# Optimization experiments

Hardware: AMD Instinct MI355X
Metric: run time of the kernel (lower is better)

## Reference

```python
import jax, jax.numpy as jnp
import numpy as np

PAD = 26
H = 1900
B = 256
T_EPI = 25
T_ANT = 64
T_TOT = 153
EMB = 10
IC = 2 * H  # classifier in_channels = 3800


def setup_inputs() -> dict:
    key = jax.random.key(0)
    ks = jax.random.split(key, 16)
    def rn(i, s, sc):
        return jax.random.normal(ks[i], s, jnp.float32) * sc
    inp = {
        "epitope_x": jax.random.randint(ks[0], (B, T_EPI), 0, 26),
        "left_antigen_x": jax.random.randint(ks[1], (B, T_ANT), 0, 26),
        "right_antigen_x": jax.random.randint(ks[2], (B, T_ANT), 0, 26),
        "total_antigen_x": jax.random.randint(ks[3], (B, T_TOT), 0, 26),
        "embed": rn(4, (27, EMB), 0.1),
        "wx": rn(5, (EMB, 4 * H), 0.1),
        "wh": rn(6, (H, 4 * H), 0.02),
        "wmx": rn(7, (EMB, H), 0.1),
        "wmh": rn(8, (H, H), 0.02),
        "b": rn(9, (4 * H,), 0.1),
        "gx": jnp.ones((4 * H,), jnp.float32),
        "gh": jnp.ones((4 * H,), jnp.float32),
        "gmx": jnp.ones((H,), jnp.float32),
        "gmh": jnp.ones((H,), jnp.float32),
        "bn1_gamma": jnp.ones((IC,), jnp.float32),
        "bn1_beta": jnp.zeros((IC,), jnp.float32),
        "bn1_mean": jnp.zeros((IC,), jnp.float32),
        "bn1_var": jnp.ones((IC,), jnp.float32),
        "W1": rn(10, (IC, IC // 10), 0.02),
        "b1": jnp.zeros((IC // 10,), jnp.float32),
        "bn2_gamma": jnp.ones((IC // 10,), jnp.float32),
        "bn2_beta": jnp.zeros((IC // 10,), jnp.float32),
        "bn2_mean": jnp.zeros((IC // 10,), jnp.float32),
        "bn2_var": jnp.ones((IC // 10,), jnp.float32),
        "W2": rn(11, (IC // 10, 1), 0.05),
        "b2": jnp.zeros((1,), jnp.float32),
    }
    return inp


def _wn(w, g):
    # tf.nn.l2_normalize(w, dim=0) * g  (eps 1e-12)
    return w * (g * jax.lax.rsqrt(jnp.maximum(jnp.sum(w * w, axis=0, keepdims=True), 1e-12)))


def _mlstm(xs, wx, wh, wmx, wmh, b):
    # xs: [T, B, E] -> hidden states [B, T, H]
    nB = xs.shape[1]
    def step(carry, x):
        c, h = carry
        m = (x @ wmx) * (h @ wmh)
        z = x @ wx + m @ wh + b
        i, f, o, u = jnp.split(z, 4, axis=1)
        c = jax.nn.sigmoid(f) * c + jax.nn.sigmoid(i) * jnp.tanh(u)
        h = jax.nn.sigmoid(o) * jnp.tanh(c)
        return (c, h), h
    init = (jnp.zeros((nB, H), xs.dtype), jnp.zeros((nB, H), xs.dtype))
    _, hs = jax.lax.scan(step, init, xs)
    return jnp.swapaxes(hs, 0, 1)


def _forward(epitope_x, left_antigen_x, right_antigen_x, total_antigen_x, embed,
             wx, wh, wmx, wmh, b, gx, gh, gmx, gmh,
             bn1_gamma, bn1_beta, bn1_mean, bn1_var, W1, b1,
             bn2_gamma, bn2_beta, bn2_mean, bn2_var, W2, b2):
    wxn = _wn(wx, gx); whn = _wn(wh, gh); wmxn = _wn(wmx, gmx); wmhn = _wn(wmh, gmh)
    epi_len = jnp.sum((epitope_x != PAD).astype(jnp.int32), axis=1)
    left_len = jnp.maximum(jnp.sum((left_antigen_x != PAD).astype(jnp.int32), axis=1), 1)
    right_len = jnp.maximum(jnp.sum((right_antigen_x != PAD).astype(jnp.int32), axis=1), 1)
    tot_len = epi_len + left_len + right_len
    epi_emb = embed[epitope_x]          # [B, 25, 10]
    tot_emb = embed[total_antigen_x]    # [B, 153, 10]
    epi_hs = _mlstm(jnp.swapaxes(epi_emb, 0, 1), wxn, whn, wmxn, wmhn, b)   # [B, 25, H]
    tot_hs = _mlstm(jnp.swapaxes(tot_emb, 0, 1), wxn, whn, wmxn, wmhn, b)   # [B, 153, H]
    ei = jnp.clip(epi_len - 1, 0, epi_hs.shape[1] - 1)
    ti = jnp.clip(tot_len - 1, 0, tot_hs.shape[1] - 1)
    epi_h = jnp.take_along_axis(epi_hs, ei[:, None, None], axis=1)[:, 0]
    tot_h = jnp.take_along_axis(tot_hs, ti[:, None, None], axis=1)[:, 0]
    x = jnp.concatenate([tot_h, epi_h], axis=-1)  # [B, 3800]
    lrelu = lambda v: jnp.where(v >= 0, v, 0.3 * v)
    bn = lambda v, g, bt, m, vv: (v - m) * jax.lax.rsqrt(vv + 1e-3) * g + bt
    x = bn(lrelu(x), bn1_gamma, bn1_beta, bn1_mean, bn1_var)
    x = x @ W1 + b1
    x = bn(lrelu(x), bn2_gamma, bn2_beta, bn2_mean, bn2_var)
    x = x @ W2 + b2
    return x.reshape(-1)


def reference(epitope_x, left_antigen_x, right_antigen_x, total_antigen_x, embed,
              wx, wh, wmx, wmh, b, gx, gh, gmx, gmh,
              bn1_gamma, bn1_beta, bn1_mean, bn1_var, W1, b1,
              bn2_gamma, bn2_beta, bn2_mean, bn2_var, W2, b2):
    return _forward(epitope_x, left_antigen_x, right_antigen_x, total_antigen_x, embed,
                    wx, wh, wmx, wmh, b, gx, gh, gmx, gmh,
                    bn1_gamma, bn1_beta, bn1_mean, bn1_var, W1, b1,
                    bn2_gamma, bn2_beta, bn2_mean, bn2_var, W2, b2)
```

## Files before the change

kernel.cpp:

```cpp
#include <hip/hip_runtime.h>


typedef _Float16 f16;
typedef _Float16 half8 __attribute__((ext_vector_type(8)));
typedef float f32x4 __attribute__((ext_vector_type(4)));

#define H_    1900
#define HP    1920
#define NKA   60
#define NKB   61
#define NKF   120
#define NR    512
#define TT    153
#define TE    25
#define EMB_  10
#define FCN   384

__device__ __forceinline__ float sigm(float x) {
  float p = __expf(-fabsf(x));
  float r = 1.f / (1.f + p);
  return x >= 0.f ? r : 1.f - r;
}
__device__ __forceinline__ float tanh_(float x) {
  float p = __expf(-2.f * fabsf(x));
  float r = (1.f - p) / (1.f + p);
  return x >= 0.f ? r : -r;
}

__device__ __forceinline__ void gll16(const f16* g, f16* l) {
  __builtin_amdgcn_global_load_lds(
      (const __attribute__((address_space(1))) unsigned int*)g,
      (__attribute__((address_space(3))) unsigned int*)l, 16, 0, 0);
}


__global__ void k_norms_p(const float* __restrict__ wh, const float* __restrict__ wx,
                          const float* __restrict__ wmh, const float* __restrict__ wmx,
                          float* __restrict__ part) {
  int seg = blockIdx.x & 3;
  int tid = (blockIdx.x >> 2) * 256 + threadIdx.x;
  float s = 0.f;
  if (tid < 7600) {
    int k0 = seg * 475;
    for (int k = k0; k < k0 + 475; k++) { float v = wh[(size_t)k * 7600 + tid]; s += v * v; }
  } else if (tid < 15200) {
    if (seg == 0) {
      int n = tid - 7600;
      for (int e = 0; e < EMB_; e++) { float v = wx[(size_t)e * 7600 + n]; s += v * v; }
    }
  } else if (tid < 17100) {
    int n = tid - 15200; int k0 = seg * 475;
    for (int k = k0; k < k0 + 475; k++) { float v = wmh[(size_t)k * H_ + n]; s += v * v; }
  } else if (tid < 19000) {
    if (seg == 0) {
      int n = tid - 17100;
      for (int e = 0; e < EMB_; e++) { float v = wmx[(size_t)e * H_ + n]; s += v * v; }
    }
  }
  if (tid < 19000) part[(size_t)seg * 19000 + tid] = s;
}

__global__ void k_norms_f(const float* __restrict__ part,
                          const float* __restrict__ gh, const float* __restrict__ gx,
                          const float* __restrict__ gmh, const float* __restrict__ gmx,
                          float* __restrict__ inv_wh, float* __restrict__ inv_wx,
                          float* __restrict__ inv_wmh, float* __restrict__ inv_wmx) {
  int tid = blockIdx.x * 256 + threadIdx.x;
  if (tid >= 19000) return;
  float s = part[tid] + part[19000 + tid] + part[38000 + tid] + part[57000 + tid];
  float r = rsqrtf(fmaxf(s, 1e-12f));
  if (tid < 7600)        inv_wh[tid] = gh[tid] * r;
  else if (tid < 15200)  { int n = tid - 7600;  inv_wx[n]  = gx[n]  * r; }
  else if (tid < 17100)  { int n = tid - 15200; inv_wmh[n] = gmh[n] * r; }
  else                   { int n = tid - 17100; inv_wmx[n] = gmx[n] * r; }
}

__global__ void k_wmhS(const float* __restrict__ wmh, const float* __restrict__ inv,
                       f16* __restrict__ WmhS) {
  int i = blockIdx.x * 256 + threadIdx.x;
  if (i >= 1920 * 1920) return;
  int n = i % 1920, k = i / 1920;
  float v = (n < H_ && k < H_) ? wmh[(size_t)k * H_ + n] * inv[n] : 0.f;
  int c = n >> 4, nl = n & 15, kb = k >> 5, kl = k & 31;
  WmhS[(((size_t)c * NKA + kb) * 512) + (nl + 16 * (kl >> 3)) * 8 + (kl & 7)] = (f16)v;
}

__global__ void k_whS(const float* __restrict__ wh, const float* __restrict__ wx,
                      const float* __restrict__ bias,
                      const float* __restrict__ inv_wh, const float* __restrict__ inv_wx,
                      f16* __restrict__ WhS) {
  int i = blockIdx.x * 256 + threadIdx.x;
  if (i >= 7600 * 1952) return;
  int col = i % 7600, k = i / 7600;
  float v = 0.f;
  if (k < H_)                        v = wh[(size_t)k * 7600 + col] * inv_wh[col];
  else if (k >= HP && k < HP + EMB_) v = wx[(size_t)(k - HP) * 7600 + col] * inv_wx[col];
  else if (k == HP + EMB_)           v = bias[col];
  int g = col / H_, n = col % H_;
  int q = n >> 4, nl = n & 15, kb = k >> 5, kl = k & 31;
  WhS[(((size_t)(q * 4 + g) * NKB + kb) * 512) + (nl + 16 * (kl >> 3)) * 8 + (kl & 7)] = (f16)v;
}

__global__ void k_wmxT(const float* __restrict__ wmx, const float* __restrict__ inv_wmx,
                       f16* __restrict__ wmxT) {
  int i = blockIdx.x * 256 + threadIdx.x;
  if (i >= HP * 32) return;
  int n = i >> 5, k = i & 31;
  float v = (k < EMB_ && n < H_) ? wmx[(size_t)k * H_ + n] * inv_wmx[n] : 0.f;
  wmxT[i] = (f16)v;
}

__global__ void k_lens(const int* __restrict__ ex, const int* __restrict__ lx,
                       const int* __restrict__ rx, int* __restrict__ sel) {
  int s = threadIdx.x;
  int el = 0; for (int i = 0; i < 25; i++) el += (ex[s * 25 + i] != 26);
  int ll = 0; for (int i = 0; i < 64; i++) ll += (lx[s * 64 + i] != 26);
  int rl = 0; for (int i = 0; i < 64; i++) rl += (rx[s * 64 + i] != 26);
  ll = ll < 1 ? 1 : ll;  rl = rl < 1 ? 1 : rl;
  int tl = el + ll + rl;
  int ti = tl - 1; ti = ti < 0 ? 0 : (ti > 152 ? 152 : ti);
  int ei = el - 1; ei = ei < 0 ? 0 : (ei > 24 ? 24 : ei);
  sel[s] = ti; sel[256 + s] = ei;
}

__global__ void k_init(f16* __restrict__ h0, f16* __restrict__ h1, float* __restrict__ c) {
  int i = blockIdx.x * 256 + threadIdx.x;
  if (i < NR * HP) { h0[i] = (f16)0.f; h1[i] = (f16)0.f; c[i] = 0.f; }
}

__global__ void k_xe16(const int* __restrict__ totx, const int* __restrict__ epix,
                       const float* __restrict__ embed, f16* __restrict__ xe16) {
  int i = blockIdx.x * blockDim.x + threadIdx.x;
  if (i >= TT * NR) return;
  int t = i / NR, r = i % NR;
  int tok = -1;
  if (r < 256) tok = totx[r * TT + t];
  else if (t < TE) tok = epix[(r - 256) * TE + t];
  f16* o = xe16 + (size_t)i * 32;
  #pragma unroll
  for (int e = 0; e < EMB_; e++) o[e] = (f16)(tok >= 0 ? embed[tok * EMB_ + e] : 0.f);
  o[10] = (f16)1.f;
  #pragma unroll
  for (int e = 11; e < 32; e++) o[e] = (f16)0.f;
}


__global__ __launch_bounds__(256, 2)
void k_stepA(const f16* __restrict__ hS, const f16* __restrict__ WmhS,
             const f16* __restrict__ xe16_t, const f16* __restrict__ wmxT,
             f16* __restrict__ mS, int rgc) {
  __shared__ __align__(16) f16 Bb[2][8][2][512];
  const int lane = threadIdx.x & 63, wid = threadIdx.x >> 6;
  const int bi = blockIdx.x;
  const int x = bi & 7, mm = bi >> 3;
  const int rg = mm % rgc, rem = mm / rgc;
  const int cbh = rem & 1, chi = rem >> 1;
  const int ct = chi * 8 + x;
  if (ct >= 30) return;
  const int rtile = rg * 4 + wid;
  const int r0 = rtile * 16;
  const int l16 = lane & 15, l4 = lane >> 4;

  const f16* Abase = hS   + (size_t)rtile * NKA * 512 + lane * 8;
  const f16* Bglob = WmhS + (size_t)(ct * 4 + cbh * 2) * NKA * 512 + lane * 8;

  f32x4 xm[2];
  {
    half8 xa = *(const half8*)(xe16_t + (size_t)(r0 + l16) * 32 + l4 * 8);
    #pragma unroll
    for (int cb = 0; cb < 2; cb++) {
      half8 xb = *(const half8*)(wmxT + (size_t)(ct * 64 + (cbh * 2 + cb) * 16 + l16) * 32 + l4 * 8);
      f32x4 z = {0.f, 0.f, 0.f, 0.f};
      xm[cb] = __builtin_amdgcn_mfma_f32_16x16x32_f16(xa, xb, z, 0, 0, 0);
    }
  }

  half8 Areg[2][8];
  f32x4 acc[2];
  #pragma unroll
  for (int cb = 0; cb < 2; cb++) { f32x4 z = {0.f, 0.f, 0.f, 0.f}; acc[cb] = z; }

#define STAGE_A(g, buf, n_) { _Pragma("unroll") for (int q_ = 0; q_ < ((n_) >> 1); q_++) { \
    int p_ = wid * ((n_) >> 1) + q_; int kbl_ = p_ >> 1, cb_ = p_ & 1; \
    gll16(Bglob + ((size_t)cb_ * NKA + (g) * 8 + kbl_) * 512, &Bb[buf][kbl_][cb_][0]); } }
#define LOADA_A(g, buf, n_) { _Pragma("unroll") for (int kk_ = 0; kk_ < 8; kk_++) if (kk_ < (n_)) \
    Areg[buf][kk_] = *(const half8*)(Abase + (size_t)((g) * 8 + kk_) * 512); }
#define COMP_A(g, buf, n_) { _Pragma("unroll") for (int kk_ = 0; kk_ < 8; kk_++) if (kk_ < (n_)) { \
    half8 b0_ = *(const half8*)&Bb[buf][kk_][0][lane * 8]; \
    half8 b1_ = *(const half8*)&Bb[buf][kk_][1][lane * 8]; \
    acc[0] = __builtin_amdgcn_mfma_f32_16x16x32_f16(Areg[buf][kk_], b0_, acc[0], 0, 0, 0); \
    acc[1] = __builtin_amdgcn_mfma_f32_16x16x32_f16(Areg[buf][kk_], b1_, acc[1], 0, 0, 0); } }

  LOADA_A(0, 0, 8); STAGE_A(0, 0, 8);
  __syncthreads();
  #pragma unroll
  for (int g = 0; g < 8; g++) {
    const int nn = (g == 7) ? 4 : 8;
    if (g < 7) {
      const int nn1 = (g == 6) ? 4 : 8;
      STAGE_A(g + 1, (g + 1) & 1, nn1); LOADA_A(g + 1, (g + 1) & 1, nn1);
    }
    COMP_A(g, g & 1, nn);
    __syncthreads();
  }
#undef STAGE_A
#undef LOADA_A
#undef COMP_A

  const int q4 = lane >> 4, c16 = lane & 15;
  const int kb = ct * 2 + cbh;
  #pragma unroll
  for (int cb = 0; cb < 2; cb++) {
    int klane = cb * 16 + c16;
    int lf = (klane >> 3) * 16;
    int sub = c16 & 7;
    f16* dst = mS + ((size_t)rtile * NKB + kb) * 512 + sub;
    #pragma unroll
    for (int q = 0; q < 4; q++) {
      int rl = q4 * 4 + q;
      dst[(rl + lf) * 8] = (f16)(acc[cb][q] * xm[cb][q]);
    }
  }
  if (ct == 0 && cbh == 0) {
    f16* dst = mS + ((size_t)rtile * NKB + 60) * 512 + lane * 8;
    *(half8*)dst = *(const half8*)(xe16_t + (size_t)(r0 + l16) * 32 + l4 * 8);
  }
}

__global__ __launch_bounds__(256, 2)
void k_stepB(const f16* __restrict__ mS, const f16* __restrict__ WhS,
             float* __restrict__ c, f16* __restrict__ houtS,
             float* __restrict__ selH, const int* __restrict__ sel, int t, int rgc) {
  __shared__ __align__(16) f16 Bb[2][4][4][512];
  const int lane = threadIdx.x & 63, wid = threadIdx.x >> 6;
  const int bi = blockIdx.x;
  const int x = bi & 7, mm = bi >> 3;
  const int rg = mm % rgc, chi = mm / rgc;
  const int colq = chi * 8 + x;
  if (colq >= 119) return;
  const int rtile = rg * 4 + wid;
  const int r0 = rtile * 16;

  const f16* Abase = mS  + (size_t)rtile * NKB * 512 + lane * 8;
  const f16* Bglob = WhS + (size_t)(colq * 4) * NKB * 512 + lane * 8;

  half8 Areg[2][4];
  f32x4 acc[4];
  #pragma unroll
  for (int b = 0; b < 4; b++) { f32x4 z = {0.f, 0.f, 0.f, 0.f}; acc[b] = z; }

#define STAGE_B(g, buf, n_) { _Pragma("unroll") for (int q_ = 0; q_ < (n_); q_++) { \
    int p_ = wid * (n_) + q_; int kbl_ = p_ >> 2, gg_ = p_ & 3; \
    gll16(Bglob + ((size_t)gg_ * NKB + (g) * 4 + kbl_) * 512, &Bb[buf][kbl_][gg_][0]); } }
#define LOADA_B(g, buf, n_) { _Pragma("unroll") for (int kk_ = 0; kk_ < 4; kk_++) if (kk_ < (n_)) \
    Areg[buf][kk_] = *(const half8*)(Abase + (size_t)((g) * 4 + kk_) * 512); }
#define COMP_B(g, buf, n_) { _Pragma("unroll") for (int kk_ = 0; kk_ < 4; kk_++) if (kk_ < (n_)) { \
    half8 b0_ = *(const half8*)&Bb[buf][kk_][0][lane * 8]; \
    half8 b1_ = *(const half8*)&Bb[buf][kk_][1][lane * 8]; \
    half8 b2_ = *(const half8*)&Bb[buf][kk_][2][lane * 8]; \
    half8 b3_ = *(const half8*)&Bb[buf][kk_][3][lane * 8]; \
    acc[0] = __builtin_amdgcn_mfma_f32_16x16x32_f16(Areg[buf][kk_], b0_, acc[0], 0, 0, 0); \
    acc[1] = __builtin_amdgcn_mfma_f32_16x16x32_f16(Areg[buf][kk_], b1_, acc[1], 0, 0, 0); \
    acc[2] = __builtin_amdgcn_mfma_f32_16x16x32_f16(Areg[buf][kk_], b2_, acc[2], 0, 0, 0); \
    acc[3] = __builtin_amdgcn_mfma_f32_16x16x32_f16(Areg[buf][kk_], b3_, acc[3], 0, 0, 0); } }

  LOADA_B(0, 0, 4); STAGE_B(0, 0, 4);
  __syncthreads();
  #pragma unroll
  for (int g = 0; g < 16; g++) {
    const int nn = (g == 15) ? 1 : 4;
    if (g < 15) {
      const int nn1 = (g == 14) ? 1 : 4;
      STAGE_B(g + 1, (g + 1) & 1, nn1); LOADA_B(g + 1, (g + 1) & 1, nn1);
    }
    COMP_B(g, g & 1, nn);
    __syncthreads();
  }
#undef STAGE_B
#undef LOADA_B
#undef COMP_B

  const int q4 = lane >> 4, c16 = lane & 15;
  const int j = colq * 16 + c16;
  const bool valid = j < H_;
  const int kbh = colq >> 1;
  const int lfh = ((((colq & 1) * 16 + c16) >> 3)) * 16;
  const int subh = c16 & 7;
  f16* hdst = houtS + ((size_t)rtile * NKA + kbh) * 512 + subh;
  #pragma unroll
  for (int q = 0; q < 4; q++) {
    int rl = q4 * 4 + q;
    int row = r0 + rl;
    if (valid) {
      size_t idx = (size_t)row * HP + j;
      float cold = c[idx];
      float iz = acc[0][q], fz = acc[1][q];
      float oz = acc[2][q], uz = acc[3][q];
      float cn = sigm(fz) * cold + sigm(iz) * tanh_(uz);
      float hv = sigm(oz) * tanh_(cn);
      c[idx] = cn;
      hdst[(rl + lfh) * 8] = (f16)hv;
      if (t == sel[row]) selH[idx] = hv;
    }
  }
}


__global__ void k_xqS(const float* __restrict__ selH, const float* __restrict__ g1,
                      const float* __restrict__ be1, const float* __restrict__ mu1,
                      const float* __restrict__ var1, f16* __restrict__ xqS) {
  int i = blockIdx.x * 256 + threadIdx.x;
  if (i >= 256 * 3840) return;
  int k = i % 3840, s = i / 3840;
  float v = 0.f; bool have = false;
  if (k < H_)            { v = selH[(size_t)s * HP + k]; have = true; }
  else if (k < 2 * H_)   { v = selH[(size_t)(256 + s) * HP + (k - H_)]; have = true; }
  float q = 0.f;
  if (have) {
    float lr = v < 0.f ? 0.3f * v : v;
    q = (lr - mu1[k]) * rsqrtf(var1[k] + 1e-3f) * g1[k] + be1[k];
  }
  int rtile = s >> 4, sl = s & 15, kb = k >> 5, kl = k & 31;
  xqS[(((size_t)rtile * NKF + kb) * 512) + (sl + 16 * (kl >> 3)) * 8 + (kl & 7)] = (f16)q;
}

__global__ void k_w1S(const float* __restrict__ W1, f16* __restrict__ W1S) {
  int i = blockIdx.x * 256 + threadIdx.x;
  if (i >= 384 * 3840) return;
  int col = i % 384, k = i / 384;
  float v = (col < 380 && k < 2 * H_) ? W1[(size_t)k * 380 + col] : 0.f;
  int cg = col >> 4, nl = col & 15, kb = k >> 5, kl = k & 31;
  W1S[(((size_t)cg * NKF + kb) * 512) + (nl + 16 * (kl >> 3)) * 8 + (kl & 7)] = (f16)v;
}

__global__ __launch_bounds__(256)
void k_fc1(const f16* __restrict__ xqS, const f16* __restrict__ W1S,
           const float* __restrict__ b1, float* __restrict__ z1) {
  const int lane = threadIdx.x & 63, wid = threadIdx.x >> 6;
  const int ct = blockIdx.x % 6, rg = blockIdx.x / 6;
  const int rtile = rg * 4 + wid;
  const int r0 = rtile * 16;

  const f16* Abase = xqS + (size_t)rtile * NKF * 512 + lane * 8;
  const f16* Bbase = W1S + (size_t)(ct * 4) * NKF * 512 + lane * 8;

  half8 fa0, fa1, fa2, fa3;
  half8 fb0[4], fb1[4], fb2[4], fb3[4];
  f32x4 acc[4];
  #pragma unroll
  for (int cb = 0; cb < 4; cb++) { f32x4 z = {0.f, 0.f, 0.f, 0.f}; acc[cb] = z; }

#define LDA_F(d, kb)  d = *(const half8*)(Abase + (size_t)(kb) * 512)
#define LDB_F(d, kb)  { _Pragma("unroll") for (int cb = 0; cb < 4; cb++) \
    d[cb] = *(const half8*)(Bbase + ((size_t)cb * NKF + (kb)) * 512); }
#define MMA_F(fa, fb) { _Pragma("unroll") for (int cb = 0; cb < 4; cb++) \
    acc[cb] = __builtin_amdgcn_mfma_f32_16x16x32_f16(fa, fb[cb], acc[cb], 0, 0, 0); }

  LDA_F(fa0, 0); LDB_F(fb0, 0);
  LDA_F(fa1, 1); LDB_F(fb1, 1);
  LDA_F(fa2, 2); LDB_F(fb2, 2);
  for (int base = 0; base < 116; base += 4) {
    LDA_F(fa3, base + 3); LDB_F(fb3, base + 3);
    MMA_F(fa0, fb0);
    LDA_F(fa0, base + 4); LDB_F(fb0, base + 4);
    MMA_F(fa1, fb1);
    LDA_F(fa1, base + 5); LDB_F(fb1, base + 5);
    MMA_F(fa2, fb2);
    LDA_F(fa2, base + 6); LDB_F(fb2, base + 6);
    MMA_F(fa3, fb3);
  }
  LDA_F(fa3, 119); LDB_F(fb3, 119);
  MMA_F(fa0, fb0);
  MMA_F(fa1, fb1);
  MMA_F(fa2, fb2);
  MMA_F(fa3, fb3);
#undef LDA_F
#undef LDB_F
#undef MMA_F

  const int q4 = lane >> 4, c16 = lane & 15;
  #pragma unroll
  for (int cb = 0; cb < 4; cb++)
    #pragma unroll
    for (int q = 0; q < 4; q++) {
      int row = r0 + q4 * 4 + q;
      int col = ct * 64 + cb * 16 + c16;
      float bias = (col < 380) ? b1[col] : 0.f;
      z1[(size_t)row * FCN + col] = acc[cb][q] + bias;
    }
}

__global__ void k_fc2(const float* __restrict__ z1, const float* __restrict__ g2,
                      const float* __restrict__ be2, const float* __restrict__ mu2,
                      const float* __restrict__ var2, const float* __restrict__ W2,
                      const float* __restrict__ b2, float* __restrict__ out) {
  int s = threadIdx.x;
  float a = 0.f;
  for (int jj = 0; jj < 380; jj++) {
    float v = z1[(size_t)s * FCN + jj];
    float lr = v < 0.f ? 0.3f * v : v;
    float q = (lr - mu2[jj]) * rsqrtf(var2[jj] + 1e-3f) * g2[jj] + be2[jj];
    a += q * W2[jj];
  }
  out[s] = a + b2[0];
}


extern "C" void kernel_launch(void* const* d_in, const int* in_sizes, int n_in,
                              void* d_out, int out_size, void* d_ws, size_t ws_size,
                              hipStream_t stream) {
  const int*   epix  = (const int*)d_in[0];
  const int*   lx    = (const int*)d_in[1];
  const int*   rx    = (const int*)d_in[2];
  const int*   totx  = (const int*)d_in[3];
  const float* embed = (const float*)d_in[4];
  const float* wx    = (const float*)d_in[5];
  const float* wh    = (const float*)d_in[6];
  const float* wmx   = (const float*)d_in[7];
  const float* wmh   = (const float*)d_in[8];
  const float* bb    = (const float*)d_in[9];
  const float* gx    = (const float*)d_in[10];
  const float* gh    = (const float*)d_in[11];
  const float* gmx   = (const float*)d_in[12];
  const float* gmh   = (const float*)d_in[13];
  const float* bn1g  = (const float*)d_in[14];
  const float* bn1b  = (const float*)d_in[15];
  const float* bn1m  = (const float*)d_in[16];
  const float* bn1v  = (const float*)d_in[17];
  const float* W1    = (const float*)d_in[18];
  const float* b1    = (const float*)d_in[19];
  const float* bn2g  = (const float*)d_in[20];
  const float* bn2b  = (const float*)d_in[21];
  const float* bn2m  = (const float*)d_in[22];
  const float* bn2v  = (const float*)d_in[23];
  const float* W2    = (const float*)d_in[24];
  const float* b2v   = (const float*)d_in[25];

  char* base = (char*)d_ws;
  size_t off = 0;
  auto alloc = [&](size_t n) { char* p = base + off; off = (off + n + 255) & ~(size_t)255; return p; };

  f16*   WmhS   = (f16*)  alloc((size_t)120 * NKA * 512 * 2);
  f16*   WhS    = (f16*)  alloc((size_t)119 * 4 * NKB * 512 * 2);
  f16*   wmxT   = (f16*)  alloc((size_t)HP * 32 * 2);
  f16*   xe16   = (f16*)  alloc((size_t)TT * NR * 32 * 2);
  f16*   h0S    = (f16*)  alloc((size_t)32 * NKA * 512 * 2);
  f16*   h1S    = (f16*)  alloc((size_t)32 * NKA * 512 * 2);
  f16*   mS     = (f16*)  alloc((size_t)32 * NKB * 512 * 2);
  float* cst    = (float*)alloc((size_t)NR * HP * 4);
  float* selH   = (float*)alloc((size_t)NR * HP * 4);
  int*   sel    = (int*)  alloc((size_t)NR * 4);
  float* inv_wh = (float*)alloc(7600 * 4);
  float* inv_wx = (float*)alloc(7600 * 4);
  float* inv_wmh= (float*)alloc(1900 * 4);
  float* inv_wmx= (float*)alloc(1900 * 4);
  float* npart  = (float*)alloc((size_t)4 * 19000 * 4);
  f16*   xqS    = (f16*)  alloc((size_t)16 * NKF * 512 * 2);
  f16*   W1S    = (f16*)  alloc((size_t)24 * NKF * 512 * 2);
  float* z1     = (float*)alloc((size_t)256 * FCN * 4);
  (void)in_sizes; (void)n_in; (void)out_size; (void)ws_size;

  hipLaunchKernelGGL(k_norms_p, dim3(300), dim3(256), 0, stream, wh, wx, wmh, wmx, npart);
  hipLaunchKernelGGL(k_norms_f, dim3(75), dim3(256), 0, stream,
                     npart, gh, gx, gmh, gmx, inv_wh, inv_wx, inv_wmh, inv_wmx);
  hipLaunchKernelGGL(k_wmhS, dim3((1920 * 1920 + 255) / 256), dim3(256), 0, stream,
                     wmh, inv_wmh, WmhS);
  hipLaunchKernelGGL(k_whS, dim3((7600 * 1952 + 255) / 256), dim3(256), 0, stream,
                     wh, wx, bb, inv_wh, inv_wx, WhS);
  hipLaunchKernelGGL(k_wmxT, dim3((HP * 32 + 255) / 256), dim3(256), 0, stream,
                     wmx, inv_wmx, wmxT);
  hipLaunchKernelGGL(k_lens, dim3(1), dim3(256), 0, stream, epix, lx, rx, sel);
  hipLaunchKernelGGL(k_init, dim3((NR * HP + 255) / 256), dim3(256), 0, stream,
                     h0S, h1S, cst);
  hipLaunchKernelGGL(k_xe16, dim3((TT * NR + 255) / 256), dim3(256), 0, stream,
                     totx, epix, embed, xe16);

  for (int t = 0; t < TT; t++) {
    int Mt = (t < TE) ? NR : 256;
    const f16* hin = (t & 1) ? h1S : h0S;
    f16*       ho  = (t & 1) ? h0S : h1S;
    int rgcA = Mt / 64;
    int rgcB = Mt / 64;
    hipLaunchKernelGGL(k_stepA, dim3(64 * rgcA), dim3(256), 0, stream,
                       hin, WmhS, xe16 + (size_t)t * NR * 32, wmxT, mS, rgcA);
    hipLaunchKernelGGL(k_stepB, dim3(8 * rgcB * 15), dim3(256), 0, stream,
                       mS, WhS, cst, ho, selH, sel, t, rgcB);
  }

  hipLaunchKernelGGL(k_xqS, dim3((256 * 3840 + 255) / 256), dim3(256), 0, stream,
                     selH, bn1g, bn1b, bn1m, bn1v, xqS);
  hipLaunchKernelGGL(k_w1S, dim3((384 * 3840 + 255) / 256), dim3(256), 0, stream, W1, W1S);
  hipLaunchKernelGGL(k_fc1, dim3(24), dim3(256), 0, stream, xqS, W1S, b1, z1);
  hipLaunchKernelGGL(k_fc2, dim3(1), dim3(256), 0, stream,
                     z1, bn2g, bn2b, bn2m, bn2v, W2, b2v, (float*)d_out);
}
```

Before: 4.308 ms.

## Store input/output gate weights as scaled FP8 to cut recurrent weight traffic

The i and o gate columns of the fused Wh/Wx/bias matrix are stored as FP8 e4m3, each with a per-column power-of-two scale taken from max-abs statistics gathered in the norm kernel. The f and u gates stay in FP16. In k_stepB the FP8 tiles are staged to LDS, converted to FP16 in registers before the MFMA, and the i/o accumulators are multiplied by the inverse scale. This lowers the bytes streamed per timestep for the largest weight, at the cost of conversion ALU work per tile and lower precision on two gates.

```diff
diff --git a/kernel.cpp b/kernel.cpp
--- a/kernel.cpp
+++ b/kernel.cpp
@@ -3,7 +3,9 @@
 
 typedef _Float16 f16;
 typedef _Float16 half8 __attribute__((ext_vector_type(8)));
+typedef __fp16 fp16x2 __attribute__((ext_vector_type(2)));
 typedef float f32x4 __attribute__((ext_vector_type(4)));
+typedef float f32x2 __attribute__((ext_vector_type(2)));
 
 #define H_    1900
 #define HP    1920
@@ -32,21 +34,32 @@
       (const __attribute__((address_space(1))) unsigned int*)g,
       (__attribute__((address_space(3))) unsigned int*)l, 16, 0, 0);
 }
+__device__ __forceinline__ void gll16b(const unsigned char* g, unsigned char* l) {
+  __builtin_amdgcn_global_load_lds(
+      (const __attribute__((address_space(1))) unsigned int*)g,
+      (__attribute__((address_space(3))) unsigned int*)l, 16, 0, 0);
+}
 
 
 __global__ void k_norms_p(const float* __restrict__ wh, const float* __restrict__ wx,
                           const float* __restrict__ wmh, const float* __restrict__ wmx,
-                          float* __restrict__ part) {
+                          float* __restrict__ part, float* __restrict__ pmax) {
   int seg = blockIdx.x & 3;
   int tid = (blockIdx.x >> 2) * 256 + threadIdx.x;
-  float s = 0.f;
+  float s = 0.f, pm = 0.f;
   if (tid < 7600) {
     int k0 = seg * 475;
-    for (int k = k0; k < k0 + 475; k++) { float v = wh[(size_t)k * 7600 + tid]; s += v * v; }
+    for (int k = k0; k < k0 + 475; k++) {
+      float v = wh[(size_t)k * 7600 + tid]; s += v * v;
+      float a = fabsf(v); pm = a > pm ? a : pm;
+    }
   } else if (tid < 15200) {
     if (seg == 0) {
       int n = tid - 7600;
-      for (int e = 0; e < EMB_; e++) { float v = wx[(size_t)e * 7600 + n]; s += v * v; }
+      for (int e = 0; e < EMB_; e++) {
+        float v = wx[(size_t)e * 7600 + n]; s += v * v;
+        float a = fabsf(v); pm = a > pm ? a : pm;
+      }
     }
   } else if (tid < 17100) {
     int n = tid - 15200; int k0 = seg * 475;
@@ -57,22 +70,38 @@
       for (int e = 0; e < EMB_; e++) { float v = wmx[(size_t)e * H_ + n]; s += v * v; }
     }
   }
-  if (tid < 19000) part[(size_t)seg * 19000 + tid] = s;
-}
-
-__global__ void k_norms_f(const float* __restrict__ part,
+  if (tid < 19000) { part[(size_t)seg * 19000 + tid] = s; pmax[(size_t)seg * 19000 + tid] = pm; }
+}
+
+__global__ void k_norms_f(const float* __restrict__ part, const float* __restrict__ pmax,
+                          const float* __restrict__ bb,
                           const float* __restrict__ gh, const float* __restrict__ gx,
                           const float* __restrict__ gmh, const float* __restrict__ gmx,
                           float* __restrict__ inv_wh, float* __restrict__ inv_wx,
-                          float* __restrict__ inv_wmh, float* __restrict__ inv_wmx) {
+                          float* __restrict__ inv_wmh, float* __restrict__ inv_wmx,
+                          float* __restrict__ cs, float* __restrict__ cinv) {
   int tid = blockIdx.x * 256 + threadIdx.x;
   if (tid >= 19000) return;
   float s = part[tid] + part[19000 + tid] + part[38000 + tid] + part[57000 + tid];
   float r = rsqrtf(fmaxf(s, 1e-12f));
-  if (tid < 7600)        inv_wh[tid] = gh[tid] * r;
-  else if (tid < 15200)  { int n = tid - 7600;  inv_wx[n]  = gx[n]  * r; }
-  else if (tid < 17100)  { int n = tid - 15200; inv_wmh[n] = gmh[n] * r; }
-  else                   { int n = tid - 17100; inv_wmx[n] = gmx[n] * r; }
+  if (tid < 7600) {
+    float iw = gh[tid] * r;
+    inv_wh[tid] = iw;
+    float mwh = fmaxf(fmaxf(pmax[tid], pmax[19000 + tid]),
+                      fmaxf(pmax[38000 + tid], pmax[57000 + tid]));
+    int txd = 7600 + tid;
+    float sx = part[txd] + part[19000 + txd] + part[38000 + txd] + part[57000 + txd];
+    float rx = rsqrtf(fmaxf(sx, 1e-12f));
+    float iwx = gx[tid] * rx;
+    float mwx = pmax[txd];
+    float cm = fmaxf(fmaxf(fabsf(iw) * mwh, fabsf(iwx) * mwx), fabsf(bb[tid]));
+    float sq = 1.f;
+    if (cm > 1e-20f) sq = exp2f(floorf(log2f(448.f / cm)));
+    cs[tid] = sq;
+    cinv[tid] = 1.f / sq;
+  } else if (tid < 15200)  { int n = tid - 7600;  inv_wx[n]  = gx[n]  * r; }
+  else if (tid < 17100)    { int n = tid - 15200; inv_wmh[n] = gmh[n] * r; }
+  else                     { int n = tid - 17100; inv_wmx[n] = gmx[n] * r; }
 }
 
 __global__ void k_wmhS(const float* __restrict__ wmh, const float* __restrict__ inv,
@@ -85,20 +114,55 @@
   WmhS[(((size_t)c * NKA + kb) * 512) + (nl + 16 * (kl >> 3)) * 8 + (kl & 7)] = (f16)v;
 }
 
-__global__ void k_whS(const float* __restrict__ wh, const float* __restrict__ wx,
-                      const float* __restrict__ bias,
-                      const float* __restrict__ inv_wh, const float* __restrict__ inv_wx,
-                      f16* __restrict__ WhS) {
-  int i = blockIdx.x * 256 + threadIdx.x;
-  if (i >= 7600 * 1952) return;
-  int col = i % 7600, k = i / 7600;
+__global__ void k_whS8io(const float* __restrict__ wh, const float* __restrict__ wx,
+                         const float* __restrict__ bias,
+                         const float* __restrict__ inv_wh, const float* __restrict__ inv_wx,
+                         const float* __restrict__ cs, unsigned char* __restrict__ Wio8) {
+  int i = blockIdx.x * 256 + threadIdx.x;
+  if (i >= 3800 * 976) return;
+  int col2 = i % 3800, kp = i / 3800;
+  int slot = col2 / 1900, n = col2 % 1900;
+  int g = slot * 2;
+  int col = g * H_ + n;
+  int k = kp * 2;
+  float sc = cs[col];
+  float v0 = 0.f, v1 = 0.f;
+  {
+    int kk = k;
+    if (kk < H_)                         v0 = wh[(size_t)kk * 7600 + col] * inv_wh[col];
+    else if (kk >= HP && kk < HP + EMB_) v0 = wx[(size_t)(kk - HP) * 7600 + col] * inv_wx[col];
+    else if (kk == HP + EMB_)            v0 = bias[col];
+  }
+  {
+    int kk = k + 1;
+    if (kk < H_)                         v1 = wh[(size_t)kk * 7600 + col] * inv_wh[col];
+    else if (kk >= HP && kk < HP + EMB_) v1 = wx[(size_t)(kk - HP) * 7600 + col] * inv_wx[col];
+    else if (kk == HP + EMB_)            v1 = bias[col];
+  }
+  int colq = n >> 4, c16 = n & 15, kb = k >> 5, kl = k & 31;
+  size_t off = ((size_t)(colq * NKB + kb)) * 1024 + (size_t)slot * 512
+             + (c16 + 16 * (kl >> 3)) * 8 + (kl & 7);
+  int r = __builtin_amdgcn_cvt_pk_fp8_f32(v0 * sc, v1 * sc, 0, false);
+  *(unsigned short*)(Wio8 + off) = (unsigned short)(r & 0xffff);
+}
+
+__global__ void k_whSfu(const float* __restrict__ wh, const float* __restrict__ wx,
+                        const float* __restrict__ bias,
+                        const float* __restrict__ inv_wh, const float* __restrict__ inv_wx,
+                        f16* __restrict__ Wfu) {
+  int i = blockIdx.x * 256 + threadIdx.x;
+  if (i >= 3800 * 1952) return;
+  int col2 = i % 3800, k = i / 3800;
+  int slot = col2 / 1900, n = col2 % 1900;
+  int g = slot * 2 + 1;
+  int col = g * H_ + n;
   float v = 0.f;
-  if (k < H_)                        v = wh[(size_t)k * 7600 + col] * inv_wh[col];
-  else if (k >= HP && k < HP + EMB_) v = wx[(size_t)(k - HP) * 7600 + col] * inv_wx[col];
-  else if (k == HP + EMB_)           v = bias[col];
-  int g = col / H_, n = col % H_;
-  int q = n >> 4, nl = n & 15, kb = k >> 5, kl = k & 31;
-  WhS[(((size_t)(q * 4 + g) * NKB + kb) * 512) + (nl + 16 * (kl >> 3)) * 8 + (kl & 7)] = (f16)v;
+  if (k < H_)                         v = wh[(size_t)k * 7600 + col] * inv_wh[col];
+  else if (k >= HP && k < HP + EMB_)  v = wx[(size_t)(k - HP) * 7600 + col] * inv_wx[col];
+  else if (k == HP + EMB_)            v = bias[col];
+  int colq = n >> 4, c16 = n & 15, kb = k >> 5, kl = k & 31;
+  Wfu[((size_t)(colq * NKB + kb)) * 1024 + (size_t)slot * 512
+      + (c16 + 16 * (kl >> 3)) * 8 + (kl & 7)] = (f16)v;
 }
 
 __global__ void k_wmxT(const float* __restrict__ wmx, const float* __restrict__ inv_wmx,
@@ -228,10 +292,12 @@
 }
 
 __global__ __launch_bounds__(256, 2)
-void k_stepB(const f16* __restrict__ mS, const f16* __restrict__ WhS,
+void k_stepB(const f16* __restrict__ mS, const unsigned char* __restrict__ Wio8,
+             const f16* __restrict__ Wfu, const float* __restrict__ cinv,
              float* __restrict__ c, f16* __restrict__ houtS,
              float* __restrict__ selH, const int* __restrict__ sel, int t, int rgc) {
-  __shared__ __align__(16) f16 Bb[2][4][4][512];
+  __shared__ __align__(16) unsigned char Bb8[2][4][1024];
+  __shared__ __align__(16) f16 Bbf[2][4][2][512];
   const int lane = threadIdx.x & 63, wid = threadIdx.x >> 6;
   const int bi = blockIdx.x;
   const int x = bi & 7, mm = bi >> 3;
@@ -241,28 +307,48 @@
   const int rtile = rg * 4 + wid;
   const int r0 = rtile * 16;
 
-  const f16* Abase = mS  + (size_t)rtile * NKB * 512 + lane * 8;
-  const f16* Bglob = WhS + (size_t)(colq * 4) * NKB * 512 + lane * 8;
+  const f16* Abase = mS + (size_t)rtile * NKB * 512 + lane * 8;
+  const unsigned char* Bio = Wio8 + (size_t)colq * NKB * 1024 + lane * 16;
+  const f16* Bfu = Wfu + (size_t)colq * NKB * 1024 + lane * 8;
 
   half8 Areg[2][4];
   f32x4 acc[4];
   #pragma unroll
   for (int b = 0; b < 4; b++) { f32x4 z = {0.f, 0.f, 0.f, 0.f}; acc[b] = z; }
 
-#define STAGE_B(g, buf, n_) { _Pragma("unroll") for (int q_ = 0; q_ < (n_); q_++) { \
-    int p_ = wid * (n_) + q_; int kbl_ = p_ >> 2, gg_ = p_ & 3; \
-    gll16(Bglob + ((size_t)gg_ * NKB + (g) * 4 + kbl_) * 512, &Bb[buf][kbl_][gg_][0]); } }
+#define STAGE_B(g, buf, n_) { _Pragma("unroll") for (int q_ = 0; q_ < 3; q_++) { \
+    int p_ = wid * 3 + q_; \
+    if (p_ < (n_) * 3) { int kbl_ = p_ / 3, u_ = p_ % 3; \
+      if (u_ == 0)      gll16b(Bio + ((size_t)((g) * 4 + kbl_)) * 1024, &Bb8[buf][kbl_][0]); \
+      else if (u_ == 1) gll16(Bfu + ((size_t)(((g) * 4 + kbl_) * 2)) * 512, &Bbf[buf][kbl_][0][0]); \
+      else              gll16(Bfu + ((size_t)(((g) * 4 + kbl_) * 2 + 1)) * 512, &Bbf[buf][kbl_][1][0]); } } }
 #define LOADA_B(g, buf, n_) { _Pragma("unroll") for (int kk_ = 0; kk_ < 4; kk_++) if (kk_ < (n_)) \
     Areg[buf][kk_] = *(const half8*)(Abase + (size_t)((g) * 4 + kk_) * 512); }
+#define CVT8(dst_, src_) { \
+    unsigned int lo_ = ((const unsigned int*)(src_))[0]; \
+    unsigned int hi_ = ((const unsigned int*)(src_))[1]; \
+    f32x2 c0_ = __builtin_amdgcn_cvt_pk_f32_fp8(lo_, false); \
+    f32x2 c1_ = __builtin_amdgcn_cvt_pk_f32_fp8(lo_, true); \
+    f32x2 c2_ = __builtin_amdgcn_cvt_pk_f32_fp8(hi_, false); \
+    f32x2 c3_ = __builtin_amdgcn_cvt_pk_f32_fp8(hi_, true); \
+    fp16x2 h0_ = __builtin_amdgcn_cvt_pkrtz(c0_.x, c0_.y); \
+    fp16x2 h1_ = __builtin_amdgcn_cvt_pkrtz(c1_.x, c1_.y); \
+    fp16x2 h2_ = __builtin_amdgcn_cvt_pkrtz(c2_.x, c2_.y); \
+    fp16x2 h3_ = __builtin_amdgcn_cvt_pkrtz(c3_.x, c3_.y); \
+    dst_[0] = (f16)h0_.x; dst_[1] = (f16)h0_.y; \
+    dst_[2] = (f16)h1_.x; dst_[3] = (f16)h1_.y; \
+    dst_[4] = (f16)h2_.x; dst_[5] = (f16)h2_.y; \
+    dst_[6] = (f16)h3_.x; dst_[7] = (f16)h3_.y; }
 #define COMP_B(g, buf, n_) { _Pragma("unroll") for (int kk_ = 0; kk_ < 4; kk_++) if (kk_ < (n_)) { \
-    half8 b0_ = *(const half8*)&Bb[buf][kk_][0][lane * 8]; \
-    half8 b1_ = *(const half8*)&Bb[buf][kk_][1][lane * 8]; \
-    half8 b2_ = *(const half8*)&Bb[buf][kk_][2][lane * 8]; \
-    half8 b3_ = *(const half8*)&Bb[buf][kk_][3][lane * 8]; \
-    acc[0] = __builtin_amdgcn_mfma_f32_16x16x32_f16(Areg[buf][kk_], b0_, acc[0], 0, 0, 0); \
-    acc[1] = __builtin_amdgcn_mfma_f32_16x16x32_f16(Areg[buf][kk_], b1_, acc[1], 0, 0, 0); \
-    acc[2] = __builtin_amdgcn_mfma_f32_16x16x32_f16(Areg[buf][kk_], b2_, acc[2], 0, 0, 0); \
-    acc[3] = __builtin_amdgcn_mfma_f32_16x16x32_f16(Areg[buf][kk_], b3_, acc[3], 0, 0, 0); } }
+    half8 bi_, bo_; \
+    CVT8(bi_, &Bb8[buf][kk_][lane * 8]); \
+    CVT8(bo_, &Bb8[buf][kk_][512 + lane * 8]); \
+    half8 bf_ = *(const half8*)&Bbf[buf][kk_][0][lane * 8]; \
+    half8 bu_ = *(const half8*)&Bbf[buf][kk_][1][lane * 8]; \
+    acc[0] = __builtin_amdgcn_mfma_f32_16x16x32_f16(Areg[buf][kk_], bi_, acc[0], 0, 0, 0); \
+    acc[1] = __builtin_amdgcn_mfma_f32_16x16x32_f16(Areg[buf][kk_], bf_, acc[1], 0, 0, 0); \
+    acc[2] = __builtin_amdgcn_mfma_f32_16x16x32_f16(Areg[buf][kk_], bo_, acc[2], 0, 0, 0); \
+    acc[3] = __builtin_amdgcn_mfma_f32_16x16x32_f16(Areg[buf][kk_], bu_, acc[3], 0, 0, 0); } }
 
   LOADA_B(0, 0, 4); STAGE_B(0, 0, 4);
   __syncthreads();
@@ -278,6 +364,7 @@
   }
 #undef STAGE_B
 #undef LOADA_B
+#undef CVT8
 #undef COMP_B
 
   const int q4 = lane >> 4, c16 = lane & 15;
@@ -286,6 +373,8 @@
   const int kbh = colq >> 1;
   const int lfh = ((((colq & 1) * 16 + c16) >> 3)) * 16;
   const int subh = c16 & 7;
+  float ci0 = 1.f, ci2 = 1.f;
+  if (valid) { ci0 = cinv[j]; ci2 = cinv[2 * H_ + j]; }
   f16* hdst = houtS + ((size_t)rtile * NKA + kbh) * 512 + subh;
   #pragma unroll
   for (int q = 0; q < 4; q++) {
@@ -294,8 +383,8 @@
     if (valid) {
       size_t idx = (size_t)row * HP + j;
       float cold = c[idx];
-      float iz = acc[0][q], fz = acc[1][q];
-      float oz = acc[2][q], uz = acc[3][q];
+      float iz = acc[0][q] * ci0, fz = acc[1][q];
+      float oz = acc[2][q] * ci2, uz = acc[3][q];
       float cn = sigm(fz) * cold + sigm(iz) * tanh_(uz);
       float hv = sigm(oz) * tanh_(cn);
       c[idx] = cn;
@@ -441,7 +530,8 @@
   auto alloc = [&](size_t n) { char* p = base + off; off = (off + n + 255) & ~(size_t)255; return p; };
 
   f16*   WmhS   = (f16*)  alloc((size_t)120 * NKA * 512 * 2);
-  f16*   WhS    = (f16*)  alloc((size_t)119 * 4 * NKB * 512 * 2);
+  unsigned char* Wio8 = (unsigned char*)alloc((size_t)119 * NKB * 1024);
+  f16*   Wfu    = (f16*)  alloc((size_t)119 * NKB * 1024 * 2);
   f16*   wmxT   = (f16*)  alloc((size_t)HP * 32 * 2);
   f16*   xe16   = (f16*)  alloc((size_t)TT * NR * 32 * 2);
   f16*   h0S    = (f16*)  alloc((size_t)32 * NKA * 512 * 2);
@@ -455,18 +545,25 @@
   float* inv_wmh= (float*)alloc(1900 * 4);
   float* inv_wmx= (float*)alloc(1900 * 4);
   float* npart  = (float*)alloc((size_t)4 * 19000 * 4);
+  float* npmax  = (float*)alloc((size_t)4 * 19000 * 4);
+  float* cs     = (float*)alloc(7600 * 4);
+  float* cinv   = (float*)alloc(7600 * 4);
   f16*   xqS    = (f16*)  alloc((size_t)16 * NKF * 512 * 2);
   f16*   W1S    = (f16*)  alloc((size_t)24 * NKF * 512 * 2);
   float* z1     = (float*)alloc((size_t)256 * FCN * 4);
   (void)in_sizes; (void)n_in; (void)out_size; (void)ws_size;
 
-  hipLaunchKernelGGL(k_norms_p, dim3(300), dim3(256), 0, stream, wh, wx, wmh, wmx, npart);
+  hipLaunchKernelGGL(k_norms_p, dim3(300), dim3(256), 0, stream,
+                     wh, wx, wmh, wmx, npart, npmax);
   hipLaunchKernelGGL(k_norms_f, dim3(75), dim3(256), 0, stream,
-                     npart, gh, gx, gmh, gmx, inv_wh, inv_wx, inv_wmh, inv_wmx);
+                     npart, npmax, bb, gh, gx, gmh, gmx,
+                     inv_wh, inv_wx, inv_wmh, inv_wmx, cs, cinv);
   hipLaunchKernelGGL(k_wmhS, dim3((1920 * 1920 + 255) / 256), dim3(256), 0, stream,
                      wmh, inv_wmh, WmhS);
-  hipLaunchKernelGGL(k_whS, dim3((7600 * 1952 + 255) / 256), dim3(256), 0, stream,
-                     wh, wx, bb, inv_wh, inv_wx, WhS);
+  hipLaunchKernelGGL(k_whS8io, dim3((3800 * 976 + 255) / 256), dim3(256), 0, stream,
+                     wh, wx, bb, inv_wh, inv_wx, cs, Wio8);
+  hipLaunchKernelGGL(k_whSfu, dim3((3800 * 1952 + 255) / 256), dim3(256), 0, stream,
+                     wh, wx, bb, inv_wh, inv_wx, Wfu);
   hipLaunchKernelGGL(k_wmxT, dim3((HP * 32 + 255) / 256), dim3(256), 0, stream,
                      wmx, inv_wmx, wmxT);
   hipLaunchKernelGGL(k_lens, dim3(1), dim3(256), 0, stream, epix, lx, rx, sel);
@@ -484,7 +581,7 @@
     hipLaunchKernelGGL(k_stepA, dim3(64 * rgcA), dim3(256), 0, stream,
                        hin, WmhS, xe16 + (size_t)t * NR * 32, wmxT, mS, rgcA);
     hipLaunchKernelGGL(k_stepB, dim3(8 * rgcB * 15), dim3(256), 0, stream,
-                       mS, WhS, cst, ho, selH, sel, t, rgcB);
+                       mS, Wio8, Wfu, cinv, cst, ho, selH, sel, t, rgcB);
   }
 
   hipLaunchKernelGGL(k_xqS, dim3((256 * 3840 + 255) / 256), dim3(256), 0, stream,
```

After: 4.923 ms. 14.3% more time.
